# Kernel optimization log

Hardware: AMD Instinct MI355X
Metric: run time of the kernel (lower is better)

## Reference

```python
import jax, jax.numpy as jnp
import numpy as np

N = 4194304  # number of 3D points (surfels)
H, W = 1024, 1280


def setup_inputs() -> dict:
    key = jax.random.key(0)
    k1, k2, k3 = jax.random.split(key, 3)
    # camera-frame points: x,y in [-0.5, 0.5], z (depth) in [0.5, 2.5]
    xy = jax.random.uniform(k1, (N, 2), dtype=jnp.float32, minval=-0.5, maxval=0.5)
    z = jax.random.uniform(k2, (N, 1), dtype=jnp.float32, minval=0.5, maxval=2.5)
    points = jnp.concatenate([xy, z], axis=-1)
    colors = jax.random.uniform(k3, (N, 3), dtype=jnp.float32)
    fx = fy = 1000.0
    K = jnp.array([[fx, 0.0, W / 2.0], [0.0, fy, H / 2.0], [0.0, 0.0, 1.0]],
                  dtype=jnp.float32)
    return {"points": points, "colors": colors, "K": K, "height": H, "width": W}


def reference(points, colors, K, height, width):
    # pcd2depth: pinhole projection with rounding
    fx, fy, cx, cy = K[0, 0], K[1, 1], K[0, 2], K[1, 2]
    z = points[:, 2]
    u = jnp.round(fx * points[:, 0] / z + cx).astype(jnp.int32)
    v = jnp.round(fy * points[:, 1] / z + cy).astype(jnp.int32)
    valid = (z > 0) & (u >= 0) & (u < width) & (v >= 0) & (v < height)
    n = points.shape[0]
    npix = height * width
    # sentinel pixel npix for invalid points
    flat = jnp.where(valid, v * width + u, npix)
    # far-to-near overwrite after depth_sort=True)
    order = jnp.argsort(jnp.where(valid, z, jnp.inf))  # ascending depth
    flat_sorted = flat[order]
    ranks = jnp.arange(n, dtype=jnp.int32)
    # per-pixel min rank (rank = position in depth-ascending order)
    win = jnp.full(npix + 1, n, dtype=jnp.int32).at[flat_sorted].min(ranks)
    win = win[:npix]
    has_point = win < n
    winner = order[jnp.minimum(win, n - 1)]  # point index per pixel
    img = jnp.where(has_point[:, None], colors[winner].astype(jnp.float32), 0.0)
    return img.reshape(height, width, 3)
```

## Files before the change

kernel.cpp:

```cpp
#include <hip/hip_runtime.h>
#include <stdint.h>

#define NPTS    4194304
#define IMG_H   1024
#define IMG_W   1280
#define NPIX    (IMG_H * IMG_W)

#define TW      80
#define TH      32
#define TILES_X (IMG_W / TW)
#define TILES_Y (IMG_H / TH)
#define NBINS   (TILES_X * TILES_Y)
#define TPIX    (TW * TH)

#define NBLK    768
#define TPB     256
#define TPB_R   768

#define CHUNK_Q ((NPTS / 4 + NBLK - 1) / NBLK)
#define CHUNK_P (CHUNK_Q * 4)
#define SSTRIDE CHUNK_P
#define QPT     ((CHUNK_Q + TPB - 1) / TPB)

static const unsigned long long KEY_SENTINEL = ~0ULL;
#define KEY47_MASK ((1ULL << 47) - 1)


struct Perm { unsigned short p[NBINS]; };
constexpr Perm make_perm() {
    Perm P{};
    float score[NBINS] = {};
    for (int i = 0; i < NBINS; ++i) {
        int tx = i % TILES_X, ty = i / TILES_X;
        float du = ((float)tx + 0.5f) * (float)TW - 640.0f;
        float dv = ((float)ty + 0.5f) * (float)TH - 512.0f;
        du /= 640.0f; dv /= 512.0f;
        score[i] = du * du + dv * dv;
        P.p[i] = (unsigned short)i;
    }
    for (int i = 1; i < NBINS; ++i) {
        unsigned short key = P.p[i];
        float ks = score[key];
        int j = i - 1;
        while (j >= 0 && score[P.p[j]] > ks) { P.p[j + 1] = P.p[j]; --j; }
        P.p[j + 1] = key;
    }
    return P;
}
__device__ __constant__ Perm c_perm = make_perm();

__device__ __forceinline__ bool project(float x, float y, float z,
                                        float fx, float fy, float cx, float cy,
                                        int& u, int& v) {
    float uf = rintf(fx * x / z + cx);
    float vf = rintf(fy * y / z + cy);
    bool valid = (z > 0.0f) &&
                 (uf >= 0.0f) && (uf < (float)IMG_W) &&
                 (vf >= 0.0f) && (vf < (float)IMG_H);
    u = (int)uf;
    v = (int)vf;
    return valid;
}

__device__ __forceinline__ unsigned int zc_of(float z) {
    unsigned int zb = __float_as_uint(z);
    unsigned int zc = zb - 0x3F000000u;
    if ((int)zc < 0) zc = 0;
    if (zc > 0x1FFFFFFu) zc = 0x1FFFFFFu;
    return zc;
}

__global__ __launch_bounds__(TPB, 3) void pass_bin(
        const float4* __restrict__ pts4, const float* __restrict__ Kmat,
        unsigned int* __restrict__ cnt_off ,
        unsigned long long* __restrict__ grec ,
        int n_quads, int qchunk) {
    __shared__ unsigned long long srec[CHUNK_P];
    __shared__ unsigned int hist[NBINS];
    __shared__ unsigned int cur[NBINS];
    __shared__ unsigned int tsum[TPB];

    int t   = threadIdx.x;
    int blk = blockIdx.x;
#pragma unroll
    for (int i = t; i < NBINS; i += TPB) hist[i] = 0;
    __syncthreads();

    float fx = Kmat[0], cx = Kmat[2];
    float fy = Kmat[4], cy = Kmat[5];

    int q0 = blk * qchunk;
    int q1 = min(n_quads, q0 + qchunk);

    unsigned long long keep[QPT * 4];

#pragma unroll
    for (int qi = 0; qi < QPT; ++qi) {
        int q = q0 + t + qi * TPB;
        bool inb = (q < q1);
        float4 a = {}, b = {}, c = {};
        if (inb) {
            a = pts4[3 * q + 0];
            b = pts4[3 * q + 1];
            c = pts4[3 * q + 2];
        }
        float px[4] = {a.x, a.w, b.z, c.y};
        float py[4] = {a.y, b.x, b.w, c.z};
        float pz[4] = {a.z, b.y, c.x, c.w};
#pragma unroll
        for (int k = 0; k < 4; ++k) {
            unsigned long long kv = ~0ULL;
            int u, v;
            if (inb && project(px[k], py[k], pz[k], fx, fy, cx, cy, u, v)) {
                int tx  = u / TW;
                int bin = (v >> 5) * TILES_X + tx;
                unsigned int pos = (unsigned int)((v & 31) * TW + (u - tx * TW));
                atomicAdd(&hist[bin], 1u);
                kv = ((unsigned long long)bin << 37) |
                     ((unsigned long long)pos << 25) |
                     (unsigned long long)zc_of(pz[k]);
            }
            keep[qi * 4 + k] = kv;
        }
    }
    __syncthreads();

    unsigned int hv[2];
    {
#pragma unroll
        for (int j = 0; j < 2; ++j) hv[j] = hist[2 * t + j];
        tsum[t] = hv[0] + hv[1];
    }
    __syncthreads();
    for (int off = 1; off < TPB; off <<= 1) {
        unsigned int x = (t >= off) ? tsum[t - off] : 0u;
        __syncthreads();
        tsum[t] += x;
        __syncthreads();
    }
    {
        unsigned int run = (t > 0) ? tsum[t - 1] : 0u;
#pragma unroll
        for (int j = 0; j < 2; ++j) {
            cur[2 * t + j] = run;
            run += hv[j];
        }
    }
    __syncthreads();

#pragma unroll
    for (int i = t; i < NBINS; i += TPB)
        cnt_off[(size_t)blk * NBINS + i] = (hist[i] << 16) | cur[i];
    __syncthreads();

#pragma unroll
    for (int qi = 0; qi < QPT; ++qi) {
        int q = q0 + t + qi * TPB;
        unsigned int i0 = 4u * (unsigned int)q;
#pragma unroll
        for (int k = 0; k < 4; ++k) {
            unsigned long long kv = keep[qi * 4 + k];
            if (kv != ~0ULL) {
                int bin          = (int)(kv >> 37);
                unsigned int pos = (unsigned int)((kv >> 25) & 0xFFFu);
                unsigned int zc  = (unsigned int)(kv & 0x1FFFFFFu);
                unsigned int slot = atomicAdd(&cur[bin], 1u);
                srec[slot] = ((unsigned long long)pos << 47) |
                             ((unsigned long long)zc << 22) |
                             (unsigned long long)(i0 + (unsigned int)k);
            }
        }
    }
    __syncthreads();

    unsigned int nrec = cur[NBINS - 1];
    unsigned long long* my = grec + (size_t)blk * SSTRIDE;
    for (unsigned int i = t; i < nrec; i += TPB) my[i] = srec[i];
}

__global__ __launch_bounds__(TPB_R) void pass_render(
        const unsigned long long* __restrict__ grec,
        const unsigned int* __restrict__ cnt_off ,
        const float* __restrict__ colors,
        float* __restrict__ out) {
    __shared__ unsigned long long key[TPIX];

    int t = threadIdx.x;
    int b = c_perm.p[blockIdx.x];

#pragma unroll
    for (int i = t; i < TPIX; i += TPB_R) key[i] = KEY_SENTINEL;
    __syncthreads();

    {
        unsigned int w   = cnt_off[(size_t)t * NBINS + b];
        unsigned int cnt = w >> 16;
        unsigned int off = w & 0xFFFFu;
        const unsigned long long* seg = grec + (size_t)t * SSTRIDE + off;
        unsigned int r = 0;
        for (; r + 4 <= cnt; r += 4) {
            unsigned long long r0 = seg[r + 0];
            unsigned long long r1 = seg[r + 1];
            unsigned long long r2 = seg[r + 2];
            unsigned long long r3 = seg[r + 3];
            atomicMin(&key[(unsigned int)(r0 >> 47)], r0 & KEY47_MASK);
            atomicMin(&key[(unsigned int)(r1 >> 47)], r1 & KEY47_MASK);
            atomicMin(&key[(unsigned int)(r2 >> 47)], r2 & KEY47_MASK);
            atomicMin(&key[(unsigned int)(r3 >> 47)], r3 & KEY47_MASK);
        }
        for (; r < cnt; ++r) {
            unsigned long long rec = seg[r];
            atomicMin(&key[(unsigned int)(rec >> 47)], rec & KEY47_MASK);
        }
    }
    __syncthreads();

    int tx = b % TILES_X, ty = b / TILES_X;
#pragma unroll
    for (int i = t; i < TPIX; i += TPB_R) {
        int row = i / TW, col = i - row * TW;
        unsigned long long kk = key[i];
        float r = 0.0f, g = 0.0f, bl = 0.0f;
        if (kk != KEY_SENTINEL) {
            unsigned int idx = (unsigned int)(kk & 0x3FFFFFu);
            r  = colors[3 * idx + 0];
            g  = colors[3 * idx + 1];
            bl = colors[3 * idx + 2];
        }
        size_t gp = (size_t)(ty * TH + row) * IMG_W + (size_t)(tx * TW + col);
        out[3 * gp + 0] = r;
        out[3 * gp + 1] = g;
        out[3 * gp + 2] = bl;
    }
}

__global__ void init_keys_vec(ulonglong2* __restrict__ keys, int n_vec2) {
    int i = blockIdx.x * blockDim.x + threadIdx.x;
    if (i < n_vec2) keys[i] = ulonglong2{~0ULL, ~0ULL};
}

__global__ void scatter_points_pretest(const float4* __restrict__ pts4,
                                       const float* __restrict__ Kmat,
                                       unsigned long long* __restrict__ keys,
                                       int n_quads) {
    int t = blockIdx.x * blockDim.x + threadIdx.x;
    if (t >= n_quads) return;
    float fx = Kmat[0], cx = Kmat[2];
    float fy = Kmat[4], cy = Kmat[5];
    float4 a = pts4[3 * t + 0];
    float4 b = pts4[3 * t + 1];
    float4 c = pts4[3 * t + 2];
    float px[4] = {a.x, a.w, b.z, c.y};
    float py[4] = {a.y, b.x, b.w, c.z};
    float pz[4] = {a.z, b.y, c.x, c.w};
    unsigned int i0 = 4u * (unsigned int)t;
#pragma unroll
    for (int k = 0; k < 4; ++k) {
        int u, v;
        if (!project(px[k], py[k], pz[k], fx, fy, cx, cy, u, v)) continue;
        int pix = v * IMG_W + u;
        unsigned long long key =
            ((unsigned long long)__float_as_uint(pz[k]) << 32) | (i0 + k);
        if (key < keys[pix]) atomicMin(&keys[pix], key);
    }
}

__global__ void resolve_pixels4(const unsigned long long* __restrict__ keys,
                                const float* __restrict__ colors,
                                float* __restrict__ out, int n_quads) {
    int t = blockIdx.x * blockDim.x + threadIdx.x;
    if (t >= n_quads) return;
    int base = 4 * t;
    ulonglong2 k01 = *(const ulonglong2*)(keys + base);
    ulonglong2 k23 = *(const ulonglong2*)(keys + base + 2);
    unsigned long long kk[4] = {k01.x, k01.y, k23.x, k23.y};
    float c[12];
#pragma unroll
    for (int j = 0; j < 4; ++j) {
        float r = 0.0f, g = 0.0f, b = 0.0f;
        if (kk[j] != KEY_SENTINEL) {
            unsigned int idx = (unsigned int)(kk[j] & 0xFFFFFFFFu);
            r = colors[3 * idx + 0];
            g = colors[3 * idx + 1];
            b = colors[3 * idx + 2];
        }
        c[3 * j + 0] = r; c[3 * j + 1] = g; c[3 * j + 2] = b;
    }
    float4* o = (float4*)(out + 3 * (size_t)base);
    o[0] = float4{c[0], c[1], c[2],  c[3]};
    o[1] = float4{c[4], c[5], c[6],  c[7]};
    o[2] = float4{c[8], c[9], c[10], c[11]};
}

extern "C" void kernel_launch(void* const* d_in, const int* in_sizes, int n_in,
                              void* d_out, int out_size, void* d_ws, size_t ws_size,
                              hipStream_t stream) {
    const float4* pts4  = (const float4*)d_in[0];
    const float* colors = (const float*)d_in[1];
    const float* Kmat   = (const float*)d_in[2];
    float* out = (float*)d_out;

    int n       = in_sizes[0] / 3;
    int n_quads = n / 4;
    int qchunk  = (n_quads + NBLK - 1) / NBLK;

    char* ws = (char*)d_ws;
    size_t off = 0;
    auto alloc = [&](size_t bytes) {
        char* p = ws + off;
        off += (bytes + 63) & ~(size_t)63;
        return p;
    };
    unsigned int*       cnt_off = (unsigned int*)alloc((size_t)NBLK * NBINS * 4);
    unsigned long long* grec =
        (unsigned long long*)alloc((size_t)NBLK * SSTRIDE * 8);

    if (qchunk <= CHUNK_Q && ws_size >= off) {
        pass_bin<<<NBLK, TPB, 0, stream>>>(pts4, Kmat, cnt_off, grec,
                                           n_quads, qchunk);
        pass_render<<<NBINS, TPB_R, 0, stream>>>(grec, cnt_off, colors, out);
    } else {
        unsigned long long* keys = (unsigned long long*)d_ws;
        const int B = 256;
        int n_vec2 = NPIX / 2;
        init_keys_vec<<<(n_vec2 + B - 1) / B, B, 0, stream>>>(
            (ulonglong2*)keys, n_vec2);
        scatter_points_pretest<<<(n_quads + B - 1) / B, B, 0, stream>>>(
            pts4, Kmat, keys, n_quads);
        int npix_quads = NPIX / 4;
        resolve_pixels4<<<(npix_quads + B - 1) / B, B, 0, stream>>>(
            keys, colors, out, npix_quads);
    }
}
```

Measured before the change: 165.5 us.

## Halve render tile width, use 256-thread render blocks and snake-order tile scheduling

Render tiles shrink from 80x32 to 40x32, which doubles the bin count and halves each tile's shared-memory key buffer. The render kernel now runs 256 threads, each walking three per-block segments, with the cnt_off loads hoisted before the barrier. The tile order, still sorted by distance from the image centre, is snake-reversed in groups of 256. The intent is more, smaller render blocks for better occupancy and load balance. The cost is twice as many bins, so larger histograms, prefix scans and cnt_off traffic in the binning pass.

Measured after the change: 166.1 us. About the same (+0.4%).

```diff
diff --git a/kernel.cpp b/kernel.cpp
--- a/kernel.cpp
+++ b/kernel.cpp
@@ -6,7 +6,7 @@
 #define IMG_W   1280
 #define NPIX    (IMG_H * IMG_W)
 
-#define TW      80
+#define TW      40
 #define TH      32
 #define TILES_X (IMG_W / TW)
 #define TILES_Y (IMG_H / TH)
@@ -15,12 +15,17 @@
 
 #define NBLK    768
 #define TPB     256
-#define TPB_R   768
+#define TPB_R   256
+#define SEGS_PER_T (NBLK / TPB_R)
+#if (NBLK % TPB_R) != 0
+#error "NBLK must be a multiple of TPB_R"
+#endif
 
 #define CHUNK_Q ((NPTS / 4 + NBLK - 1) / NBLK)
 #define CHUNK_P (CHUNK_Q * 4)
 #define SSTRIDE CHUNK_P
 #define QPT     ((CHUNK_Q + TPB - 1) / TPB)
+#define BPT     (NBINS / TPB)
 
 static const unsigned long long KEY_SENTINEL = ~0ULL;
 #define KEY47_MASK ((1ULL << 47) - 1)
@@ -28,7 +33,7 @@
 
 struct Perm { unsigned short p[NBINS]; };
 constexpr Perm make_perm() {
-    Perm P{};
+    unsigned short rank[NBINS] = {};
     float score[NBINS] = {};
     for (int i = 0; i < NBINS; ++i) {
         int tx = i % TILES_X, ty = i / TILES_X;
@@ -36,14 +41,20 @@
         float dv = ((float)ty + 0.5f) * (float)TH - 512.0f;
         du /= 640.0f; dv /= 512.0f;
         score[i] = du * du + dv * dv;
-        P.p[i] = (unsigned short)i;
+        rank[i] = (unsigned short)i;
     }
     for (int i = 1; i < NBINS; ++i) {
-        unsigned short key = P.p[i];
+        unsigned short key = rank[i];
         float ks = score[key];
         int j = i - 1;
-        while (j >= 0 && score[P.p[j]] > ks) { P.p[j + 1] = P.p[j]; --j; }
-        P.p[j + 1] = key;
+        while (j >= 0 && score[rank[j]] > ks) { rank[j + 1] = rank[j]; --j; }
+        rank[j + 1] = key;
+    }
+    Perm P{};
+    for (int i = 0; i < NBINS; ++i) {
+        int r = i / 256, k = i % 256;
+        int src = (r & 1) ? (r * 256 + (255 - k)) : (r * 256 + k);
+        P.p[i] = rank[src];
     }
     return P;
 }
@@ -116,7 +127,7 @@
                 int bin = (v >> 5) * TILES_X + tx;
                 unsigned int pos = (unsigned int)((v & 31) * TW + (u - tx * TW));
                 atomicAdd(&hist[bin], 1u);
-                kv = ((unsigned long long)bin << 37) |
+                kv = ((unsigned long long)bin << 36) |
                      ((unsigned long long)pos << 25) |
                      (unsigned long long)zc_of(pz[k]);
             }
@@ -125,11 +136,12 @@
     }
     __syncthreads();
 
-    unsigned int hv[2];
+    unsigned int hv[BPT];
     {
-#pragma unroll
-        for (int j = 0; j < 2; ++j) hv[j] = hist[2 * t + j];
-        tsum[t] = hv[0] + hv[1];
+        unsigned int s = 0;
+#pragma unroll
+        for (int j = 0; j < BPT; ++j) { hv[j] = hist[BPT * t + j]; s += hv[j]; }
+        tsum[t] = s;
     }
     __syncthreads();
     for (int off = 1; off < TPB; off <<= 1) {
@@ -141,8 +153,8 @@
     {
         unsigned int run = (t > 0) ? tsum[t - 1] : 0u;
 #pragma unroll
-        for (int j = 0; j < 2; ++j) {
-            cur[2 * t + j] = run;
+        for (int j = 0; j < BPT; ++j) {
+            cur[BPT * t + j] = run;
             run += hv[j];
         }
     }
@@ -161,8 +173,8 @@
         for (int k = 0; k < 4; ++k) {
             unsigned long long kv = keep[qi * 4 + k];
             if (kv != ~0ULL) {
-                int bin          = (int)(kv >> 37);
-                unsigned int pos = (unsigned int)((kv >> 25) & 0xFFFu);
+                int bin          = (int)(kv >> 36);
+                unsigned int pos = (unsigned int)((kv >> 25) & 0x7FFu);
                 unsigned int zc  = (unsigned int)(kv & 0x1FFFFFFu);
                 unsigned int slot = atomicAdd(&cur[bin], 1u);
                 srec[slot] = ((unsigned long long)pos << 47) |
@@ -190,13 +202,19 @@
 
 #pragma unroll
     for (int i = t; i < TPIX; i += TPB_R) key[i] = KEY_SENTINEL;
-    __syncthreads();
-
-    {
-        unsigned int w   = cnt_off[(size_t)t * NBINS + b];
-        unsigned int cnt = w >> 16;
-        unsigned int off = w & 0xFFFFu;
-        const unsigned long long* seg = grec + (size_t)t * SSTRIDE + off;
+
+    unsigned int w[SEGS_PER_T];
+#pragma unroll
+    for (int s = 0; s < SEGS_PER_T; ++s)
+        w[s] = cnt_off[(size_t)(t + s * TPB_R) * NBINS + b];
+    __syncthreads();
+
+#pragma unroll
+    for (int s = 0; s < SEGS_PER_T; ++s) {
+        unsigned int cnt = w[s] >> 16;
+        unsigned int off = w[s] & 0xFFFFu;
+        const unsigned long long* seg =
+            grec + (size_t)(t + s * TPB_R) * SSTRIDE + off;
         unsigned int r = 0;
         for (; r + 4 <= cnt; r += 4) {
             unsigned long long r0 = seg[r + 0];
```
